# Kernel tuning notes

Measured on AMD Instinct MI355X. Metric: run time of the kernel, lower is better.

## Reference

```python
import jax, jax.numpy as jnp
import numpy as np

DECAY = 0.99
EPS = 1e-5  # Laplace smoothing eps in cluster-size balancing


def _quantize(z_flat, embedding, cluster_size, emb_avg, n_codes):
    # z_flat: [N, D]; embedding: [K, D]
    d = (jnp.sum(z_flat * z_flat, axis=1, keepdims=True)
         + jnp.sum(embedding * embedding, axis=1)
         - 2.0 * (z_flat @ embedding.T))                      # [N, K]
    idx = jnp.argmin(d, axis=1)                               # [N]
    # EMA update (training path). segment_sum == one-hot matmul scatter-add.
    counts = jax.ops.segment_sum(jnp.ones(z_flat.shape[0], z_flat.dtype), idx,
                                 num_segments=n_codes)        # [K]
    new_cs = cluster_size * DECAY + (1.0 - DECAY) * counts
    dw = jax.ops.segment_sum(z_flat, idx, num_segments=n_codes)  # [K, D]
    new_avg = emb_avg * DECAY + (1.0 - DECAY) * dw
    n = new_cs.sum()
    bal = (new_cs + EPS) / (n + n_codes * EPS) * n
    # torch assigns via .data (no autograd) -> stop_gradient for faithfulness
    new_emb = jax.lax.stop_gradient(new_avg / bal[:, None])
    z_q = jnp.take(new_emb, idx, axis=0)  # == one_hot(idx) @ new_emb
    return idx, z_q


def _l2norm(x):
    # F.normalize(x, dim=-1) with eps=1e-12
    return x / jnp.maximum(jnp.linalg.norm(x, axis=-1, keepdims=True), 1e-12)


def reference(z, structure_embedding, style_embedding,
              structure_cluster_size, style_cluster_size,
              structure_embedding_avg, style_embedding_avg):
    b, c, h, w, d = z.shape
    zp = jnp.transpose(z, (0, 2, 3, 4, 1))      # b h w d c
    z_flat = zp.reshape(-1, c)                  # [N, D]
    s_idx, s_q = _quantize(z_flat, structure_embedding, structure_cluster_size,
                           structure_embedding_avg, structure_embedding.shape[0])
    y_idx, y_q = _quantize(z_flat, style_embedding, style_cluster_size,
                           style_embedding_avg, style_embedding.shape[0])

    def back(q):  # [N, C] -> b c h w d
        return jnp.transpose(q.reshape(b, h, w, d, c), (0, 4, 1, 2, 3))

    s_enc = back(s_q)
    y_enc = back(y_q)
    # NOTE: faithful to source — normalize over LAST axis of (b,c,h,w,d),
    # i.e. the spatial depth axis, exactly as F.normalize(dim=-1) does there.
    dis = jnp.mean(jnp.sum(_l2norm(s_enc) * _l2norm(y_enc), axis=-1) ** 2)
    z_q = (s_enc + y_enc) * 0.5
    return z_q, dis, s_idx, y_idx


def setup_inputs() -> dict:
    key = jax.random.key(0)
    k1, k2, k3 = jax.random.split(key, 3)
    B, C, H, W, D = 16, 256, 16, 16, 16
    Ks, Ky = 1024, 512
    return {
        "z": jax.random.normal(k1, (B, C, H, W, D), dtype=jnp.float32),
        "structure_embedding": jax.random.normal(k2, (Ks, C), dtype=jnp.float32),
        "style_embedding": jax.random.normal(k3, (Ky, C), dtype=jnp.float32),
        "structure_cluster_size": jnp.zeros((Ks,), jnp.float32),
        "style_cluster_size": jnp.zeros((Ky,), jnp.float32),
        "structure_embedding_avg": jnp.zeros((Ks, C), jnp.float32),
        "style_embedding_avg": jnp.zeros((Ky, C), jnp.float32),
    }
```

## Files before the change

### kernel.cpp

```cpp
#include <hip/hip_runtime.h>
#include <float.h>

#define NROWS 65536
#define CDIM  256
#define KS    1024
#define KY    512
#define KTOT  1536
#define SPB   4096

#define WB_CNT_S       0
#define WB_CNT_Y       4096
#define WB_RESCUE_CNT  6144
#define WB_DISACC      6152
#define WB_DW_S        6400
#define WB_DW_Y        1054976
#define WB_ZERO_BYTES  1579264
#define WB_EIMG        1579264
#define WB_EN2         2365696
#define WB_IDXS_I      2371840
#define WB_IDXY_I      2633984
#define WB_RLIST_S     2896128
#define WB_RLIST_Y     3158272
#define WB_BASE_S      3420416
#define WB_BASE_Y      3424512
#define WB_CUR_S       3426560
#define WB_CUR_Y       3430656
#define WB_SCALE_S     3432704
#define WB_SCALE_Y     3436800
#define WB_PERM_S      3438848
#define WB_PERM_Y      3700992
#define WB_KSORT_S     3963136
#define WB_KSORT_Y     4225280
#define WB_PS0         4487424
#define WB_PS1         5011712

#define OFF_OUT_ZQ   0
#define OFF_OUT_DIS  16777216
#define OFF_OUT_SIDX 16777217
#define OFF_OUT_YIDX 16842753

typedef __attribute__((ext_vector_type(8)))  _Float16 f16x8;
typedef __attribute__((ext_vector_type(4)))  float    f32x4;

__device__ __forceinline__ unsigned int umn(unsigned int a, unsigned int b) { return a < b ? a : b; }
__device__ __forceinline__ unsigned int umx(unsigned int a, unsigned int b) { return a > b ? a : b; }

__global__ void prep_e(const float* __restrict__ Es, const float* __restrict__ Ey,
                       unsigned short* __restrict__ eimg, float* __restrict__ en2) {
    int wave = threadIdx.x >> 6, lane = threadIdx.x & 63;
    int k = blockIdx.x * 4 + wave;
    const float* E = (k < KS) ? (Es + (size_t)k * CDIM) : (Ey + (size_t)(k - KS) * CDIM);
    float4 v = *(const float4*)(E + lane * 4);
    float nrm = v.x * v.x + v.y * v.y + v.z * v.z + v.w * v.w;
#pragma unroll
    for (int off = 32; off > 0; off >>= 1) nrm += __shfl_down(nrm, off);
    if (lane == 0) en2[k] = nrm;

    unsigned short q0 = __builtin_bit_cast(unsigned short, (_Float16)v.x);
    unsigned short q1 = __builtin_bit_cast(unsigned short, (_Float16)v.y);
    unsigned short q2 = __builtin_bit_cast(unsigned short, (_Float16)v.z);
    unsigned short q3 = __builtin_bit_cast(unsigned short, (_Float16)v.w);
    uint2 hp = make_uint2((unsigned)q0 | ((unsigned)q1 << 16),
                          (unsigned)q2 | ((unsigned)q3 << 16));
    int c0 = lane * 4;
    int kc = c0 >> 5, g = (c0 >> 3) & 3, j0 = c0 & 7;
    size_t byteoff = (size_t)(k >> 4) * 8192 + (size_t)kc * 1024
                   + (size_t)(g * 16 + (k & 15)) * 16 + (size_t)j0 * 2;
    *(uint2*)((char*)eimg + byteoff) = hp;
}

__device__ __forceinline__ void stage1(const unsigned short* __restrict__ eimg,
                                       int chunk, char* lds, int wave, int lane) {
    const char* gs = (const char*)eimg + (size_t)chunk * 8192 + wave * 2048 + lane * 16;
    char* ls = lds + wave * 2048;
    __builtin_amdgcn_global_load_lds(
        (const __attribute__((address_space(1))) void*)gs,
        (__attribute__((address_space(3))) void*)ls, 16, 0, 0);
    __builtin_amdgcn_global_load_lds(
        (const __attribute__((address_space(1))) void*)(gs + 1024),
        (__attribute__((address_space(3))) void*)(ls + 1024), 16, 0, 0);
}

#define WAITV(n)                                                               \
    asm volatile("s_waitcnt vmcnt(" #n ")");                                   \
    __builtin_amdgcn_sched_barrier(0);

#define PSFLUSH(dst)                                                           \
    {                                                                          \
        _Pragma("unroll")                                                      \
        for (int rg = 0; rg < 2; ++rg)                                         \
        _Pragma("unroll")                                                      \
        for (int q = 0; q < 4; ++q) {                                          \
            unsigned int v1 = m1a[rg][q], v2 = m2a[rg][q];                     \
            _Pragma("unroll")                                                  \
            for (int m = 8; m >= 1; m >>= 1) {                                 \
                unsigned int o1 = (unsigned int)__shfl_xor((int)v1, m);        \
                unsigned int o2 = (unsigned int)__shfl_xor((int)v2, m);        \
                v2 = umn(umn(v2, o2), umx(v1, o1));                            \
                v1 = umn(v1, o1);                                              \
            }                                                                  \
            if ((lane & 15) == 0) {                                            \
                int n = n0 + rg * 16 + (lane >> 4) * 4 + q;                    \
                dst[n] = make_uint2(v1, v2);                                   \
            }                                                                  \
            m1a[rg][q] = 0xFFFFFFFFu; m2a[rg][q] = 0xFFFFFFFFu;                \
        }                                                                      \
    }

#define FLUSHY()                                                               \
    {                                                                          \
        _Pragma("unroll")                                                      \
        for (int rg = 0; rg < 2; ++rg)                                         \
        _Pragma("unroll")                                                      \
        for (int q = 0; q < 4; ++q) {                                          \
            unsigned int v1 = m1a[rg][q], v2 = m2a[rg][q];                     \
            _Pragma("unroll")                                                  \
            for (int m = 8; m >= 1; m >>= 1) {                                 \
                unsigned int o1 = (unsigned int)__shfl_xor((int)v1, m);        \
                unsigned int o2 = (unsigned int)__shfl_xor((int)v2, m);        \
                v2 = umn(umn(v2, o2), umx(v1, o1));                            \
                v1 = umn(v1, o1);                                              \
            }                                                                  \
            if ((lane & 15) == 0) {                                            \
                int kw = (int)(v1 & 0x7FFu) - KS;                              \
                int n = n0 + rg * 16 + (lane >> 4) * 4 + q;                    \
                yidx_f[n] = (float)kw;                                         \
                yidx_i[n] = kw;                                                \
                atomicAdd(&cnt_y[kw], 1);                                      \
                if ((v1 >> 11) + 4 > (v2 >> 11)) {                             \
                    int k2w = (int)(v2 & 0x7FFu) - KS;                         \
                    int pp = atomicAdd(&rescue_cnt[1], 1);                     \
                    if (pp < 65536) rlist_y[pp] = n | (k2w << 16);             \
                }                                                              \
            }                                                                  \
        }                                                                      \
    }

__launch_bounds__(256, 4)
__global__ void main1_kernel(const float* __restrict__ z, const unsigned short* __restrict__ eimg,
                             const float* __restrict__ en2g, float* __restrict__ zf,
                             uint2* __restrict__ ps0, uint2* __restrict__ ps1,
                             float* __restrict__ yidx_f, int* __restrict__ yidx_i,
                             int* __restrict__ cnt_y, int* __restrict__ rescue_cnt,
                             int* __restrict__ rlist_y) {
    __shared__ char lds_raw[38912];

    if (blockIdx.x < 1024) {
        char (*sh)[8192] = (char(*)[8192])lds_raw;
        float* en2l = (float*)(lds_raw + 32768);
        const int tid = threadIdx.x, wave = tid >> 6, lane = tid & 63;
        const int half = blockIdx.x & 1;
        const int n0 = (blockIdx.x >> 1) * 128 + wave * 32;
        const int cb = half * 48;

        for (int i = tid; i < KTOT; i += 256) en2l[i] = en2g[i];

        const int b = n0 >> 12;
        const int sb = (n0 & 4095) + (lane & 15);
        const float* zb = z + (size_t)b * CDIM * SPB;
        const int g8 = (lane >> 4) * 8;
        f16x8 A[2][8];
#pragma unroll
        for (int rg = 0; rg < 2; ++rg) {
#pragma unroll
            for (int kc = 0; kc < 8; ++kc) {
                f16x8 a;
#pragma unroll
                for (int j = 0; j < 8; ++j)
                    a[j] = (_Float16)zb[(size_t)(g8 + kc * 32 + j) * SPB + sb + rg * 16];
                A[rg][kc] = a;
            }
        }

        unsigned int m1a[2][4], m2a[2][4];
#pragma unroll
        for (int rg = 0; rg < 2; ++rg)
#pragma unroll
            for (int q = 0; q < 4; ++q) { m1a[rg][q] = 0xFFFFFFFFu; m2a[rg][q] = 0xFFFFFFFFu; }

        stage1(eimg, cb + 0, &sh[0][0], wave, lane);
        stage1(eimg, cb + 1, &sh[1][0], wave, lane);
        stage1(eimg, cb + 2, &sh[2][0], wave, lane);
        __syncthreads();

#pragma unroll 1
        for (int i = 0; i < 48; ++i) {
            if (i < 46)       { WAITV(4); }
            else if (i == 46) { WAITV(2); }
            else              { WAITV(0); }
            __builtin_amdgcn_s_barrier();
            asm volatile("" ::: "memory");
            if (i + 3 < 48) stage1(eimg, cb + i + 3, &sh[(i + 3) & 3][0], wave, lane);

            const int chunk = cb + i;
            const char* bb = &sh[i & 3][0] + lane * 16;
            f32x4 acc0 = {}, acc1 = {};
#pragma unroll
            for (int kc = 0; kc < 8; ++kc) {
                f16x8 B = *(const f16x8*)(bb + kc * 1024);
                acc0 = __builtin_amdgcn_mfma_f32_16x16x32_f16(A[0][kc], B, acc0, 0, 0, 0);
                acc1 = __builtin_amdgcn_mfma_f32_16x16x32_f16(A[1][kc], B, acc1, 0, 0, 0);
            }
            const int kcode = chunk * 16 + (lane & 15);
            const float en0 = en2l[kcode] + 512.0f;
            const unsigned int tag = (unsigned int)kcode;
#pragma unroll
            for (int q = 0; q < 4; ++q) {
                float d0 = fmaf(-2.f, acc0[q], en0);
                unsigned int du0 = (__float_as_uint(d0) & 0xFFFFF800u) | tag;
                m2a[0][q] = umn(m2a[0][q], umx(m1a[0][q], du0));
                m1a[0][q] = umn(m1a[0][q], du0);
                float d1 = fmaf(-2.f, acc1[q], en0);
                unsigned int du1 = (__float_as_uint(d1) & 0xFFFFF800u) | tag;
                m2a[1][q] = umn(m2a[1][q], umx(m1a[1][q], du1));
                m1a[1][q] = umn(m1a[1][q], du1);
            }

            if (half == 1 && i == 15) PSFLUSH(ps1);
        }

        if (half == 0) { PSFLUSH(ps0); }
        else           { FLUSHY(); }
    } else {
        float (*Zs)[257] = (float(*)[257])lds_raw;
        int blk = blockIdx.x - 1024;
        int n0 = blk * 32, b = n0 >> 12, s0 = n0 & 4095;
        int t = threadIdx.x;
        const float* zb = z + (size_t)b * CDIM * SPB + s0;
#pragma unroll
        for (int i = 0; i < 32; ++i) {
            int l = i * 256 + t;
            int c = l >> 5, s = l & 31;
            Zs[s][c] = zb[(size_t)c * SPB + s];
        }
        __syncthreads();
#pragma unroll
        for (int j = 0; j < 8; ++j) {
            int gid = j * 256 + t;
            int nl = gid >> 6, fg = gid & 63;
            float4 v = *(const float4*)(&Zs[nl][fg * 4]);
            *(float4*)(&zf[(size_t)(n0 + nl) * 256 + fg * 4]) = v;
        }
    }
}

__global__ void merge_s_kernel(const uint2* __restrict__ ps0, const uint2* __restrict__ ps1,
                               float* __restrict__ sidx_f, int* __restrict__ sidx_i,
                               int* __restrict__ cnt_s, int* __restrict__ rescue_cnt,
                               int* __restrict__ rlist_s) {
    int n = blockIdx.x * 256 + threadIdx.x;
    uint2 a = ps0[n], b = ps1[n];
    unsigned int v1 = umn(a.x, b.x);
    unsigned int v2 = umn(umn(a.y, b.y), umx(a.x, b.x));
    int kw = (int)(v1 & 0x7FFu);
    sidx_f[n] = (float)kw;
    sidx_i[n] = kw;
    atomicAdd(&cnt_s[kw], 1);
    if ((v1 >> 11) + 4 > (v2 >> 11)) {
        int k2w = (int)(v2 & 0x7FFu);
        int pp = atomicAdd(&rescue_cnt[0], 1);
        if (pp < 65536) rlist_s[pp] = n | (k2w << 16);
    }
}

__global__ void rescue2_kernel(const float* __restrict__ zf,
                               const float* __restrict__ Es, const float* __restrict__ Ey,
                               const float* __restrict__ en2, const int* __restrict__ rcnt,
                               const int* __restrict__ rlist_s, const int* __restrict__ rlist_y,
                               float* __restrict__ sidx_f, float* __restrict__ yidx_f,
                               int* __restrict__ sidx_i, int* __restrict__ yidx_i,
                               int* __restrict__ cnt_s, int* __restrict__ cnt_y) {
    int cs = rcnt[0]; if (cs > 65536) cs = 65536;
    int cy = rcnt[1]; if (cy > 65536) cy = 65536;
    int total = cs + cy;
    const int lane = threadIdx.x & 63;
    const int nw = (gridDim.x * blockDim.x) >> 6;
    for (int e = (int)((blockIdx.x * blockDim.x + threadIdx.x) >> 6); e < total; e += nw) {
        int book = (e >= cs);
        unsigned int ent = (unsigned int)(book ? rlist_y[e - cs] : rlist_s[e]);
        int n  = (int)(ent & 0xFFFFu);
        int k2 = (int)(ent >> 16);
        int* idx_i = book ? yidx_i : sidx_i;
        float* idx_f = book ? yidx_f : sidx_f;
        int* cnt = book ? cnt_y : cnt_s;
        const float* E = book ? Ey : Es;
        const float* en2k = book ? (en2 + KS) : en2;
        int k1 = idx_i[n];
        float4 zv = *(const float4*)(zf + (size_t)n * 256 + lane * 4);
        float4 a  = *(const float4*)(E + (size_t)k1 * 256 + lane * 4);
        float4 c  = *(const float4*)(E + (size_t)k2 * 256 + lane * 4);
        float d1 = zv.x * a.x + zv.y * a.y + zv.z * a.z + zv.w * a.w;
        float d2 = zv.x * c.x + zv.y * c.y + zv.z * c.z + zv.w * c.w;
#pragma unroll
        for (int off = 32; off > 0; off >>= 1) {
            d1 += __shfl_down(d1, off);
            d2 += __shfl_down(d2, off);
        }
        if (lane == 0) {
            float dist1 = en2k[k1] - 2.f * d1;
            float dist2 = en2k[k2] - 2.f * d2;
            int nk = (dist2 < dist1 || (dist2 == dist1 && k2 < k1)) ? k2 : k1;
            if (nk != k1) {
                atomicSub(&cnt[k1], 1);
                atomicAdd(&cnt[nk], 1);
                idx_i[n] = nk;
                idx_f[n] = (float)nk;
            }
        }
    }
}

__global__ void scanbal_kernel(const float* __restrict__ cs_in, const float* __restrict__ cy_in,
                               const int* __restrict__ cnt_s, const int* __restrict__ cnt_y,
                               int* __restrict__ base_s, int* __restrict__ base_y,
                               int* __restrict__ cur_s, int* __restrict__ cur_y,
                               float* __restrict__ scale_s, float* __restrict__ scale_y) {
    __shared__ int   sc[1024];
    __shared__ float sf[1024];
    int K = blockIdx.x ? KY : KS;
    const float* csi = blockIdx.x ? cy_in : cs_in;
    const int*   cnt = blockIdx.x ? cnt_y : cnt_s;
    int* base = blockIdx.x ? base_y : base_s;
    int* cur  = blockIdx.x ? cur_y  : cur_s;
    float* scale = blockIdx.x ? scale_y : scale_s;
    int t = threadIdx.x;
    int c = (t < K) ? cnt[t] : 0;
    float ncs = (t < K) ? (csi[t] * 0.99f + 0.01f * (float)c) : 0.f;
    sc[t] = c;
    __syncthreads();
    for (int off = 1; off < 1024; off <<= 1) {
        int v = sc[t] + ((t >= off) ? sc[t - off] : 0);
        __syncthreads();
        sc[t] = v;
        __syncthreads();
    }
    int incl = sc[t];
    sf[t] = ncs;
    __syncthreads();
    for (int s2 = 512; s2 > 0; s2 >>= 1) {
        if (t < s2) sf[t] += sf[t + s2];
        __syncthreads();
    }
    float nsum = sf[0];
    if (t < K) {
        base[t] = incl - c;
        cur[t]  = incl - c;
        float bal = (ncs + 1e-5f) / (nsum + (float)K * 1e-5f) * nsum;
        scale[t] = 1.0f / bal;
    }
}

__global__ void scatter_kernel(const int* __restrict__ si, const int* __restrict__ yi,
                               int* __restrict__ cur_s, int* __restrict__ cur_y,
                               int* __restrict__ perm_s, int* __restrict__ perm_y,
                               int* __restrict__ ksort_s, int* __restrict__ ksort_y) {
    int i = blockIdx.x * 256 + threadIdx.x;
    if (i < NROWS) {
        int k = si[i]; int p = atomicAdd(&cur_s[k], 1);
        perm_s[p] = i; ksort_s[p] = k;
    } else {
        int n = i - NROWS; int k = yi[n]; int p = atomicAdd(&cur_y[k], 1);
        perm_y[p] = n; ksort_y[p] = k;
    }
}

__global__ void dw_kernel(const float* __restrict__ zf,
                          const int* __restrict__ perm_s, const int* __restrict__ ksort_s,
                          const int* __restrict__ perm_y, const int* __restrict__ ksort_y,
                          float* __restrict__ dw_s, float* __restrict__ dw_y) {
    __shared__ int keys[65];
    __shared__ int rows[64];
    const int t = threadIdx.x;
    int blk = blockIdx.x;
    const int* perm; const int* ks; float* dw; int p0;
    if (blk < NROWS / 64) { perm = perm_s; ks = ksort_s; dw = dw_s; p0 = blk * 64; }
    else                  { perm = perm_y; ks = ksort_y; dw = dw_y; p0 = (blk - NROWS / 64) * 64; }
    if (t < 64) { keys[t] = ks[p0 + t]; rows[t] = perm[p0 + t]; }
    if (t == 64) keys[64] = -1;
    __syncthreads();
    float acc = 0.f;
#pragma unroll 8
    for (int j = 0; j < 64; ++j) {
        acc += zf[(size_t)rows[j] * 256 + t];
        if (keys[j + 1] != keys[j]) {
            atomicAdd(&dw[(size_t)keys[j] * 256 + t], acc);
            acc = 0.f;
        }
    }
}

__global__ void gather_kernel(const float* __restrict__ avg_s, const float* __restrict__ avg_y,
                              const float* __restrict__ dw_s, const float* __restrict__ dw_y,
                              const float* __restrict__ scale_s, const float* __restrict__ scale_y,
                              const int* __restrict__ sidx, const int* __restrict__ yidx,
                              float* __restrict__ zq, float* __restrict__ disacc) {
    __shared__ float qb[256 * 17];
    __shared__ int   si[16], yi[16];
    __shared__ float scs[16], scy[16];
    __shared__ float red[256];
    const int g  = blockIdx.x;
    const int b  = g >> 8;
    const int hw = g & 255;
    const int t  = threadIdx.x;
    if (t < 16) {
        int n = b * SPB + hw * 16 + t;
        int k = sidx[n];
        si[t] = k;
        scs[t] = scale_s[k];
    } else if (t < 32) {
        int n = b * SPB + hw * 16 + (t - 16);
        int k = yidx[n];
        yi[t - 16] = k;
        scy[t - 16] = scale_y[k];
    }
    __syncthreads();
    float ns = 0.f, ny = 0.f, dot = 0.f;
#pragma unroll
    for (int d = 0; d < 16; ++d) {
        size_t so = (size_t)si[d] * CDIM + t;
        size_t yo = (size_t)yi[d] * CDIM + t;
        float s = fmaf(0.01f, dw_s[so], avg_s[so] * 0.99f) * scs[d];
        float y = fmaf(0.01f, dw_y[yo], avg_y[yo] * 0.99f) * scy[d];
        ns  = fmaf(s, s, ns);
        ny  = fmaf(y, y, ny);
        dot = fmaf(s, y, dot);
        qb[t * 17 + d] = 0.5f * (s + y);
    }
    float den = fmaxf(sqrtf(ns), 1e-12f) * fmaxf(sqrtf(ny), 1e-12f);
    float val = dot / den;
    red[t] = val * val;
    __syncthreads();
    for (int s = 128; s > 0; s >>= 1) {
        if (t < s) red[t] += red[t + s];
        __syncthreads();
    }
    if (t == 0) atomicAdd(disacc, red[0]);
    float* zg = zq + (size_t)b * CDIM * SPB + hw * 16;
#pragma unroll
    for (int j = 0; j < 16; ++j) {
        int e = j * 256 + t;
        int c = e >> 4, d = e & 15;
        zg[(size_t)c * SPB + d] = qb[c * 17 + d];
    }
}

__global__ void fin_kernel(const float* __restrict__ disacc, float* __restrict__ out_dis) {
    *out_dis = *disacc * (1.0f / 1048576.0f);
}

extern "C" void kernel_launch(void* const* d_in, const int* in_sizes, int n_in,
                              void* d_out, int out_size, void* d_ws, size_t ws_size,
                              hipStream_t stream) {
    const float* z     = (const float*)d_in[0];
    const float* Es    = (const float*)d_in[1];
    const float* Ey    = (const float*)d_in[2];
    const float* s_cs  = (const float*)d_in[3];
    const float* y_cs  = (const float*)d_in[4];
    const float* s_avg = (const float*)d_in[5];
    const float* y_avg = (const float*)d_in[6];
    float* out = (float*)d_out;
    char*  w   = (char*)d_ws;

    unsigned short* eimg = (unsigned short*)(w + WB_EIMG);
    float* en2    = (float*)(w + WB_EN2);
    int* idxs_i   = (int*)(w + WB_IDXS_I);
    int* idxy_i   = (int*)(w + WB_IDXY_I);
    int* cnt_s    = (int*)(w + WB_CNT_S);
    int* cnt_y    = (int*)(w + WB_CNT_Y);
    int* r_cnt    = (int*)(w + WB_RESCUE_CNT);
    int* rlist_s  = (int*)(w + WB_RLIST_S);
    int* rlist_y  = (int*)(w + WB_RLIST_Y);
    int* base_s   = (int*)(w + WB_BASE_S);
    int* base_y   = (int*)(w + WB_BASE_Y);
    int* cur_s    = (int*)(w + WB_CUR_S);
    int* cur_y    = (int*)(w + WB_CUR_Y);
    float* scale_s = (float*)(w + WB_SCALE_S);
    float* scale_y = (float*)(w + WB_SCALE_Y);
    int* perm_s   = (int*)(w + WB_PERM_S);
    int* perm_y   = (int*)(w + WB_PERM_Y);
    int* ksort_s  = (int*)(w + WB_KSORT_S);
    int* ksort_y  = (int*)(w + WB_KSORT_Y);
    float* dw_s   = (float*)(w + WB_DW_S);
    float* dw_y   = (float*)(w + WB_DW_Y);
    uint2* ps0    = (uint2*)(w + WB_PS0);
    uint2* ps1    = (uint2*)(w + WB_PS1);

    float* zf     = out + OFF_OUT_ZQ;
    float* sidx_f = out + OFF_OUT_SIDX;
    float* yidx_f = out + OFF_OUT_YIDX;

    hipMemsetAsync(w, 0, WB_ZERO_BYTES, stream);

    prep_e<<<384, 256, 0, stream>>>(Es, Ey, eimg, en2);

    main1_kernel<<<1024 + 2048, 256, 0, stream>>>(
        z, eimg, en2, zf, ps0, ps1, yidx_f, idxy_i, cnt_y, r_cnt, rlist_y);

    merge_s_kernel<<<NROWS / 256, 256, 0, stream>>>(ps0, ps1, sidx_f, idxs_i,
                                                    cnt_s, r_cnt, rlist_s);

    rescue2_kernel<<<512, 256, 0, stream>>>(zf, Es, Ey, en2, r_cnt, rlist_s, rlist_y,
                                            sidx_f, yidx_f, idxs_i, idxy_i, cnt_s, cnt_y);

    scanbal_kernel<<<2, 1024, 0, stream>>>(s_cs, y_cs, cnt_s, cnt_y, base_s, base_y,
                                           cur_s, cur_y, scale_s, scale_y);
    scatter_kernel<<<2 * NROWS / 256, 256, 0, stream>>>(idxs_i, idxy_i, cur_s, cur_y,
                                                        perm_s, perm_y, ksort_s, ksort_y);
    dw_kernel<<<2 * NROWS / 64, 256, 0, stream>>>(zf, perm_s, ksort_s, perm_y, ksort_y, dw_s, dw_y);
    gather_kernel<<<4096, 256, 0, stream>>>(s_avg, y_avg, dw_s, dw_y, scale_s, scale_y,
                                            idxs_i, idxy_i,
                                            out + OFF_OUT_ZQ, (float*)(w + WB_DISACC));
    fin_kernel<<<1, 1, 0, stream>>>((float*)(w + WB_DISACC), out + OFF_OUT_DIS);
}
```

Measured before the change: 305.1 us.

## Fuse post-argmin stages into one persistent kernel with software grid barriers

Merges the merge, rescue, scan/balance, scatter, dw accumulation, gather and finalize kernels into a single persistent tail kernel of 1024 blocks. A hand-written atomic grid barrier separates the stages, and the scan/balance step now uses 256 threads with per-thread chunks. The aim is to remove several kernel launch gaps and tail-drain bubbles. In exchange, grid-wide spin barriers add latency and require all 1024 blocks to be co-resident, and grid-stride loops replace full-occupancy launches.

```diff
diff --git a/kernel.cpp b/kernel.cpp
--- a/kernel.cpp
+++ b/kernel.cpp
@@ -12,6 +12,7 @@
 #define WB_CNT_Y       4096
 #define WB_RESCUE_CNT  6144
 #define WB_DISACC      6152
+#define WB_GBAR        6160
 #define WB_DW_S        6400
 #define WB_DW_Y        1054976
 #define WB_ZERO_BYTES  1579264
@@ -21,8 +22,6 @@
 #define WB_IDXY_I      2633984
 #define WB_RLIST_S     2896128
 #define WB_RLIST_Y     3158272
-#define WB_BASE_S      3420416
-#define WB_BASE_Y      3424512
 #define WB_CUR_S       3426560
 #define WB_CUR_Y       3430656
 #define WB_SCALE_S     3432704
@@ -244,208 +243,233 @@
     }
 }
 
-__global__ void merge_s_kernel(const uint2* __restrict__ ps0, const uint2* __restrict__ ps1,
-                               float* __restrict__ sidx_f, int* __restrict__ sidx_i,
-                               int* __restrict__ cnt_s, int* __restrict__ rescue_cnt,
-                               int* __restrict__ rlist_s) {
-    int n = blockIdx.x * 256 + threadIdx.x;
-    uint2 a = ps0[n], b = ps1[n];
-    unsigned int v1 = umn(a.x, b.x);
-    unsigned int v2 = umn(umn(a.y, b.y), umx(a.x, b.x));
-    int kw = (int)(v1 & 0x7FFu);
-    sidx_f[n] = (float)kw;
-    sidx_i[n] = kw;
-    atomicAdd(&cnt_s[kw], 1);
-    if ((v1 >> 11) + 4 > (v2 >> 11)) {
-        int k2w = (int)(v2 & 0x7FFu);
-        int pp = atomicAdd(&rescue_cnt[0], 1);
-        if (pp < 65536) rlist_s[pp] = n | (k2w << 16);
-    }
+#define TB_GRID 1024
+__device__ __forceinline__ void gbar(int* cnt, int* gen) {
+    __syncthreads();
+    if (threadIdx.x == 0) {
+        int g = __hip_atomic_load(gen, __ATOMIC_RELAXED, __HIP_MEMORY_SCOPE_AGENT);
+        int v = __hip_atomic_fetch_add(cnt, 1, __ATOMIC_ACQ_REL, __HIP_MEMORY_SCOPE_AGENT);
+        if (v == TB_GRID - 1) {
+            __hip_atomic_store(cnt, 0, __ATOMIC_RELAXED, __HIP_MEMORY_SCOPE_AGENT);
+            __hip_atomic_fetch_add(gen, 1, __ATOMIC_ACQ_REL, __HIP_MEMORY_SCOPE_AGENT);
+        } else {
+            while (__hip_atomic_load(gen, __ATOMIC_ACQUIRE, __HIP_MEMORY_SCOPE_AGENT) == g)
+                __builtin_amdgcn_s_sleep(16);
+        }
+    }
+    __syncthreads();
 }
 
-__global__ void rescue2_kernel(const float* __restrict__ zf,
-                               const float* __restrict__ Es, const float* __restrict__ Ey,
-                               const float* __restrict__ en2, const int* __restrict__ rcnt,
-                               const int* __restrict__ rlist_s, const int* __restrict__ rlist_y,
-                               float* __restrict__ sidx_f, float* __restrict__ yidx_f,
-                               int* __restrict__ sidx_i, int* __restrict__ yidx_i,
-                               int* __restrict__ cnt_s, int* __restrict__ cnt_y) {
-    int cs = rcnt[0]; if (cs > 65536) cs = 65536;
-    int cy = rcnt[1]; if (cy > 65536) cy = 65536;
-    int total = cs + cy;
-    const int lane = threadIdx.x & 63;
-    const int nw = (gridDim.x * blockDim.x) >> 6;
-    for (int e = (int)((blockIdx.x * blockDim.x + threadIdx.x) >> 6); e < total; e += nw) {
-        int book = (e >= cs);
-        unsigned int ent = (unsigned int)(book ? rlist_y[e - cs] : rlist_s[e]);
-        int n  = (int)(ent & 0xFFFFu);
-        int k2 = (int)(ent >> 16);
-        int* idx_i = book ? yidx_i : sidx_i;
-        float* idx_f = book ? yidx_f : sidx_f;
-        int* cnt = book ? cnt_y : cnt_s;
-        const float* E = book ? Ey : Es;
-        const float* en2k = book ? (en2 + KS) : en2;
-        int k1 = idx_i[n];
-        float4 zv = *(const float4*)(zf + (size_t)n * 256 + lane * 4);
-        float4 a  = *(const float4*)(E + (size_t)k1 * 256 + lane * 4);
-        float4 c  = *(const float4*)(E + (size_t)k2 * 256 + lane * 4);
-        float d1 = zv.x * a.x + zv.y * a.y + zv.z * a.z + zv.w * a.w;
-        float d2 = zv.x * c.x + zv.y * c.y + zv.z * c.z + zv.w * c.w;
-#pragma unroll
-        for (int off = 32; off > 0; off >>= 1) {
-            d1 += __shfl_down(d1, off);
-            d2 += __shfl_down(d2, off);
-        }
-        if (lane == 0) {
-            float dist1 = en2k[k1] - 2.f * d1;
-            float dist2 = en2k[k2] - 2.f * d2;
-            int nk = (dist2 < dist1 || (dist2 == dist1 && k2 < k1)) ? k2 : k1;
-            if (nk != k1) {
-                atomicSub(&cnt[k1], 1);
-                atomicAdd(&cnt[nk], 1);
-                idx_i[n] = nk;
-                idx_f[n] = (float)nk;
-            }
-        }
-    }
-}
-
-__global__ void scanbal_kernel(const float* __restrict__ cs_in, const float* __restrict__ cy_in,
-                               const int* __restrict__ cnt_s, const int* __restrict__ cnt_y,
-                               int* __restrict__ base_s, int* __restrict__ base_y,
-                               int* __restrict__ cur_s, int* __restrict__ cur_y,
-                               float* __restrict__ scale_s, float* __restrict__ scale_y) {
-    __shared__ int   sc[1024];
-    __shared__ float sf[1024];
-    int K = blockIdx.x ? KY : KS;
-    const float* csi = blockIdx.x ? cy_in : cs_in;
-    const int*   cnt = blockIdx.x ? cnt_y : cnt_s;
-    int* base = blockIdx.x ? base_y : base_s;
-    int* cur  = blockIdx.x ? cur_y  : cur_s;
-    float* scale = blockIdx.x ? scale_y : scale_s;
-    int t = threadIdx.x;
-    int c = (t < K) ? cnt[t] : 0;
-    float ncs = (t < K) ? (csi[t] * 0.99f + 0.01f * (float)c) : 0.f;
-    sc[t] = c;
-    __syncthreads();
-    for (int off = 1; off < 1024; off <<= 1) {
-        int v = sc[t] + ((t >= off) ? sc[t - off] : 0);
+struct TailArgs {
+    const float *zf_r, *Es, *Ey, *en2, *s_cs, *y_cs, *avg_s, *avg_y;
+    const uint2 *ps0, *ps1;
+    float *sidx_f, *yidx_f;
+    int *idxs_i, *idxy_i, *cnt_s, *cnt_y, *r_cnt, *rlist_s, *rlist_y;
+    int *cur_s, *cur_y;
+    float *scale_s, *scale_y;
+    int *perm_s, *perm_y, *ksort_s, *ksort_y;
+    float *dw_s, *dw_y, *zq, *disacc, *out_dis;
+    int *bar;
+};
+
+__launch_bounds__(256, 4)
+__global__ void tail_kernel(TailArgs a) {
+    __shared__ __align__(16) char smem[18688];
+    const int bid = blockIdx.x, t = threadIdx.x;
+    int* bcnt = a.bar;
+    int* bgen = a.bar + 1;
+
+    for (int n = bid * 256 + t; n < NROWS; n += TB_GRID * 256) {
+        uint2 pa = a.ps0[n], pb = a.ps1[n];
+        unsigned int v1 = umn(pa.x, pb.x);
+        unsigned int v2 = umn(umn(pa.y, pb.y), umx(pa.x, pb.x));
+        int kw = (int)(v1 & 0x7FFu);
+        a.sidx_f[n] = (float)kw;
+        a.idxs_i[n] = kw;
+        atomicAdd(&a.cnt_s[kw], 1);
+        if ((v1 >> 11) + 4 > (v2 >> 11)) {
+            int k2w = (int)(v2 & 0x7FFu);
+            int pp = atomicAdd(&a.r_cnt[0], 1);
+            if (pp < 65536) a.rlist_s[pp] = n | (k2w << 16);
+        }
+    }
+    gbar(bcnt, bgen);
+
+    {
+        int cs = a.r_cnt[0]; if (cs > 65536) cs = 65536;
+        int cy = a.r_cnt[1]; if (cy > 65536) cy = 65536;
+        int total = cs + cy;
+        const int lane = t & 63;
+        for (int e = bid * 4 + (t >> 6); e < total; e += TB_GRID * 4) {
+            int book = (e >= cs);
+            unsigned int ent = (unsigned int)(book ? a.rlist_y[e - cs] : a.rlist_s[e]);
+            int n  = (int)(ent & 0xFFFFu);
+            int k2 = (int)(ent >> 16);
+            int* idx_i = book ? a.idxy_i : a.idxs_i;
+            float* idx_f = book ? a.yidx_f : a.sidx_f;
+            int* cnt = book ? a.cnt_y : a.cnt_s;
+            const float* E = book ? a.Ey : a.Es;
+            const float* en2k = book ? (a.en2 + KS) : a.en2;
+            int k1 = idx_i[n];
+            float4 zv = *(const float4*)(a.zf_r + (size_t)n * 256 + lane * 4);
+            float4 ea = *(const float4*)(E + (size_t)k1 * 256 + lane * 4);
+            float4 ec = *(const float4*)(E + (size_t)k2 * 256 + lane * 4);
+            float d1 = zv.x * ea.x + zv.y * ea.y + zv.z * ea.z + zv.w * ea.w;
+            float d2 = zv.x * ec.x + zv.y * ec.y + zv.z * ec.z + zv.w * ec.w;
+#pragma unroll
+            for (int off = 32; off > 0; off >>= 1) {
+                d1 += __shfl_down(d1, off);
+                d2 += __shfl_down(d2, off);
+            }
+            if (lane == 0) {
+                float dist1 = en2k[k1] - 2.f * d1;
+                float dist2 = en2k[k2] - 2.f * d2;
+                int nk = (dist2 < dist1 || (dist2 == dist1 && k2 < k1)) ? k2 : k1;
+                if (nk != k1) {
+                    atomicSub(&cnt[k1], 1);
+                    atomicAdd(&cnt[nk], 1);
+                    idx_i[n] = nk;
+                    idx_f[n] = (float)nk;
+                }
+            }
+        }
+    }
+    gbar(bcnt, bgen);
+
+    if (bid < 2) {
+        int*   sdI = (int*)smem;
+        float* sdF = (float*)(smem + 1024);
+        const int K = bid ? KY : KS;
+        const int E = K >> 8;
+        const float* csi = bid ? a.y_cs : a.s_cs;
+        const int*   cnt = bid ? a.cnt_y : a.cnt_s;
+        int* cur = bid ? a.cur_y : a.cur_s;
+        float* scale = bid ? a.scale_y : a.scale_s;
+        int cl[4] = {0, 0, 0, 0};
+        float nl[4] = {0.f, 0.f, 0.f, 0.f};
+        int isum = 0; float fsum = 0.f;
+#pragma unroll
+        for (int e = 0; e < 4; ++e) {
+            if (e < E) {
+                int c = cnt[t * E + e];
+                float ncs = csi[t * E + e] * 0.99f + 0.01f * (float)c;
+                cl[e] = c; nl[e] = ncs; isum += c; fsum += ncs;
+            }
+        }
+        sdI[t] = isum; sdF[t] = fsum;
         __syncthreads();
-        sc[t] = v;
-        __syncthreads();
-    }
-    int incl = sc[t];
-    sf[t] = ncs;
-    __syncthreads();
-    for (int s2 = 512; s2 > 0; s2 >>= 1) {
-        if (t < s2) sf[t] += sf[t + s2];
-        __syncthreads();
-    }
-    float nsum = sf[0];
-    if (t < K) {
-        base[t] = incl - c;
-        cur[t]  = incl - c;
-        float bal = (ncs + 1e-5f) / (nsum + (float)K * 1e-5f) * nsum;
-        scale[t] = 1.0f / bal;
-    }
-}
-
-__global__ void scatter_kernel(const int* __restrict__ si, const int* __restrict__ yi,
-                               int* __restrict__ cur_s, int* __restrict__ cur_y,
-                               int* __restrict__ perm_s, int* __restrict__ perm_y,
-                               int* __restrict__ ksort_s, int* __restrict__ ksort_y) {
-    int i = blockIdx.x * 256 + threadIdx.x;
-    if (i < NROWS) {
-        int k = si[i]; int p = atomicAdd(&cur_s[k], 1);
-        perm_s[p] = i; ksort_s[p] = k;
-    } else {
-        int n = i - NROWS; int k = yi[n]; int p = atomicAdd(&cur_y[k], 1);
-        perm_y[p] = n; ksort_y[p] = k;
-    }
-}
-
-__global__ void dw_kernel(const float* __restrict__ zf,
-                          const int* __restrict__ perm_s, const int* __restrict__ ksort_s,
-                          const int* __restrict__ perm_y, const int* __restrict__ ksort_y,
-                          float* __restrict__ dw_s, float* __restrict__ dw_y) {
-    __shared__ int keys[65];
-    __shared__ int rows[64];
-    const int t = threadIdx.x;
-    int blk = blockIdx.x;
-    const int* perm; const int* ks; float* dw; int p0;
-    if (blk < NROWS / 64) { perm = perm_s; ks = ksort_s; dw = dw_s; p0 = blk * 64; }
-    else                  { perm = perm_y; ks = ksort_y; dw = dw_y; p0 = (blk - NROWS / 64) * 64; }
-    if (t < 64) { keys[t] = ks[p0 + t]; rows[t] = perm[p0 + t]; }
-    if (t == 64) keys[64] = -1;
-    __syncthreads();
-    float acc = 0.f;
+        for (int off = 1; off < 256; off <<= 1) {
+            int v = sdI[t] + ((t >= off) ? sdI[t - off] : 0);
+            float f = sdF[t] + ((t >= off) ? sdF[t - off] : 0.f);
+            __syncthreads();
+            sdI[t] = v; sdF[t] = f;
+            __syncthreads();
+        }
+        float nsum = sdF[255];
+        int run = sdI[t] - isum;
+#pragma unroll
+        for (int e = 0; e < 4; ++e) {
+            if (e < E) {
+                cur[t * E + e] = run;
+                float bal = (nl[e] + 1e-5f) / (nsum + (float)K * 1e-5f) * nsum;
+                scale[t * E + e] = 1.0f / bal;
+                run += cl[e];
+            }
+        }
+    }
+    gbar(bcnt, bgen);
+
+    for (int i = bid * 256 + t; i < 2 * NROWS; i += TB_GRID * 256) {
+        if (i < NROWS) {
+            int k = a.idxs_i[i]; int p = atomicAdd(&a.cur_s[k], 1);
+            a.perm_s[p] = i; a.ksort_s[p] = k;
+        } else {
+            int n = i - NROWS; int k = a.idxy_i[n]; int p = atomicAdd(&a.cur_y[k], 1);
+            a.perm_y[p] = n; a.ksort_y[p] = k;
+        }
+    }
+    gbar(bcnt, bgen);
+
+    {
+        int* keys = (int*)smem;
+        int* rows = keys + 65;
+        for (int vb = bid; vb < 2048; vb += TB_GRID) {
+            const int* perm; const int* ks; float* dwp; int p0;
+            if (vb < 1024) { perm = a.perm_s; ks = a.ksort_s; dwp = a.dw_s; p0 = vb * 64; }
+            else           { perm = a.perm_y; ks = a.ksort_y; dwp = a.dw_y; p0 = (vb - 1024) * 64; }
+            __syncthreads();
+            if (t < 64) { keys[t] = ks[p0 + t]; rows[t] = perm[p0 + t]; }
+            if (t == 64) keys[64] = -1;
+            __syncthreads();
+            float acc = 0.f;
 #pragma unroll 8
-    for (int j = 0; j < 64; ++j) {
-        acc += zf[(size_t)rows[j] * 256 + t];
-        if (keys[j + 1] != keys[j]) {
-            atomicAdd(&dw[(size_t)keys[j] * 256 + t], acc);
-            acc = 0.f;
-        }
-    }
-}
-
-__global__ void gather_kernel(const float* __restrict__ avg_s, const float* __restrict__ avg_y,
-                              const float* __restrict__ dw_s, const float* __restrict__ dw_y,
-                              const float* __restrict__ scale_s, const float* __restrict__ scale_y,
-                              const int* __restrict__ sidx, const int* __restrict__ yidx,
-                              float* __restrict__ zq, float* __restrict__ disacc) {
-    __shared__ float qb[256 * 17];
-    __shared__ int   si[16], yi[16];
-    __shared__ float scs[16], scy[16];
-    __shared__ float red[256];
-    const int g  = blockIdx.x;
-    const int b  = g >> 8;
-    const int hw = g & 255;
-    const int t  = threadIdx.x;
-    if (t < 16) {
-        int n = b * SPB + hw * 16 + t;
-        int k = sidx[n];
-        si[t] = k;
-        scs[t] = scale_s[k];
-    } else if (t < 32) {
-        int n = b * SPB + hw * 16 + (t - 16);
-        int k = yidx[n];
-        yi[t - 16] = k;
-        scy[t - 16] = scale_y[k];
-    }
-    __syncthreads();
-    float ns = 0.f, ny = 0.f, dot = 0.f;
-#pragma unroll
-    for (int d = 0; d < 16; ++d) {
-        size_t so = (size_t)si[d] * CDIM + t;
-        size_t yo = (size_t)yi[d] * CDIM + t;
-        float s = fmaf(0.01f, dw_s[so], avg_s[so] * 0.99f) * scs[d];
-        float y = fmaf(0.01f, dw_y[yo], avg_y[yo] * 0.99f) * scy[d];
-        ns  = fmaf(s, s, ns);
-        ny  = fmaf(y, y, ny);
-        dot = fmaf(s, y, dot);
-        qb[t * 17 + d] = 0.5f * (s + y);
-    }
-    float den = fmaxf(sqrtf(ns), 1e-12f) * fmaxf(sqrtf(ny), 1e-12f);
-    float val = dot / den;
-    red[t] = val * val;
-    __syncthreads();
-    for (int s = 128; s > 0; s >>= 1) {
-        if (t < s) red[t] += red[t + s];
-        __syncthreads();
-    }
-    if (t == 0) atomicAdd(disacc, red[0]);
-    float* zg = zq + (size_t)b * CDIM * SPB + hw * 16;
-#pragma unroll
-    for (int j = 0; j < 16; ++j) {
-        int e = j * 256 + t;
-        int c = e >> 4, d = e & 15;
-        zg[(size_t)c * SPB + d] = qb[c * 17 + d];
-    }
-}
-
-__global__ void fin_kernel(const float* __restrict__ disacc, float* __restrict__ out_dis) {
-    *out_dis = *disacc * (1.0f / 1048576.0f);
+            for (int j = 0; j < 64; ++j) {
+                acc += a.zf_r[(size_t)rows[j] * 256 + t];
+                if (keys[j + 1] != keys[j]) {
+                    atomicAdd(&dwp[(size_t)keys[j] * 256 + t], acc);
+                    acc = 0.f;
+                }
+            }
+        }
+    }
+    gbar(bcnt, bgen);
+
+    {
+        float* qb  = (float*)smem;
+        int*   si  = (int*)(smem + 17408);
+        int*   yi  = si + 16;
+        float* scs = (float*)(yi + 16);
+        float* scy = scs + 16;
+        float* red = scy + 16;
+        for (int g = bid; g < 4096; g += TB_GRID) {
+            __syncthreads();
+            const int b  = g >> 8;
+            const int hw = g & 255;
+            if (t < 16) {
+                int n = b * SPB + hw * 16 + t;
+                int k = a.idxs_i[n];
+                si[t] = k;
+                scs[t] = a.scale_s[k];
+            } else if (t < 32) {
+                int n = b * SPB + hw * 16 + (t - 16);
+                int k = a.idxy_i[n];
+                yi[t - 16] = k;
+                scy[t - 16] = a.scale_y[k];
+            }
+            __syncthreads();
+            float ns = 0.f, ny = 0.f, dot = 0.f;
+#pragma unroll
+            for (int d = 0; d < 16; ++d) {
+                size_t so = (size_t)si[d] * CDIM + t;
+                size_t yo = (size_t)yi[d] * CDIM + t;
+                float s = fmaf(0.01f, a.dw_s[so], a.avg_s[so] * 0.99f) * scs[d];
+                float y = fmaf(0.01f, a.dw_y[yo], a.avg_y[yo] * 0.99f) * scy[d];
+                ns  = fmaf(s, s, ns);
+                ny  = fmaf(y, y, ny);
+                dot = fmaf(s, y, dot);
+                qb[t * 17 + d] = 0.5f * (s + y);
+            }
+            float den = fmaxf(sqrtf(ns), 1e-12f) * fmaxf(sqrtf(ny), 1e-12f);
+            float val = dot / den;
+            red[t] = val * val;
+            __syncthreads();
+            for (int s = 128; s > 0; s >>= 1) {
+                if (t < s) red[t] += red[t + s];
+                __syncthreads();
+            }
+            if (t == 0) atomicAdd(a.disacc, red[0]);
+            float* zg = a.zq + (size_t)b * CDIM * SPB + hw * 16;
+#pragma unroll
+            for (int j = 0; j < 16; ++j) {
+                int e = j * 256 + t;
+                int c = e >> 4, d = e & 15;
+                zg[(size_t)c * SPB + d] = qb[c * 17 + d];
+            }
+        }
+    }
+    gbar(bcnt, bgen);
+
+    if (bid == 0 && t == 0) *a.out_dis = *a.disacc * (1.0f / 1048576.0f);
 }
 
 extern "C" void kernel_launch(void* const* d_in, const int* in_sizes, int n_in,
@@ -463,52 +487,49 @@
 
     unsigned short* eimg = (unsigned short*)(w + WB_EIMG);
     float* en2    = (float*)(w + WB_EN2);
-    int* idxs_i   = (int*)(w + WB_IDXS_I);
-    int* idxy_i   = (int*)(w + WB_IDXY_I);
-    int* cnt_s    = (int*)(w + WB_CNT_S);
-    int* cnt_y    = (int*)(w + WB_CNT_Y);
-    int* r_cnt    = (int*)(w + WB_RESCUE_CNT);
-    int* rlist_s  = (int*)(w + WB_RLIST_S);
-    int* rlist_y  = (int*)(w + WB_RLIST_Y);
-    int* base_s   = (int*)(w + WB_BASE_S);
-    int* base_y   = (int*)(w + WB_BASE_Y);
-    int* cur_s    = (int*)(w + WB_CUR_S);
-    int* cur_y    = (int*)(w + WB_CUR_Y);
-    float* scale_s = (float*)(w + WB_SCALE_S);
-    float* scale_y = (float*)(w + WB_SCALE_Y);
-    int* perm_s   = (int*)(w + WB_PERM_S);
-    int* perm_y   = (int*)(w + WB_PERM_Y);
-    int* ksort_s  = (int*)(w + WB_KSORT_S);
-    int* ksort_y  = (int*)(w + WB_KSORT_Y);
-    float* dw_s   = (float*)(w + WB_DW_S);
-    float* dw_y   = (float*)(w + WB_DW_Y);
-    uint2* ps0    = (uint2*)(w + WB_PS0);
-    uint2* ps1    = (uint2*)(w + WB_PS1);
-
     float* zf     = out + OFF_OUT_ZQ;
-    float* sidx_f = out + OFF_OUT_SIDX;
-    float* yidx_f = out + OFF_OUT_YIDX;
 
     hipMemsetAsync(w, 0, WB_ZERO_BYTES, stream);
 
     prep_e<<<384, 256, 0, stream>>>(Es, Ey, eimg, en2);
 
     main1_kernel<<<1024 + 2048, 256, 0, stream>>>(
-        z, eimg, en2, zf, ps0, ps1, yidx_f, idxy_i, cnt_y, r_cnt, rlist_y);
-
-    merge_s_kernel<<<NROWS / 256, 256, 0, stream>>>(ps0, ps1, sidx_f, idxs_i,
-                                                    cnt_s, r_cnt, rlist_s);
-
-    rescue2_kernel<<<512, 256, 0, stream>>>(zf, Es, Ey, en2, r_cnt, rlist_s, rlist_y,
-                                            sidx_f, yidx_f, idxs_i, idxy_i, cnt_s, cnt_y);
-
-    scanbal_kernel<<<2, 1024, 0, stream>>>(s_cs, y_cs, cnt_s, cnt_y, base_s, base_y,
-                                           cur_s, cur_y, scale_s, scale_y);
-    scatter_kernel<<<2 * NROWS / 256, 256, 0, stream>>>(idxs_i, idxy_i, cur_s, cur_y,
-                                                        perm_s, perm_y, ksort_s, ksort_y);
-    dw_kernel<<<2 * NROWS / 64, 256, 0, stream>>>(zf, perm_s, ksort_s, perm_y, ksort_y, dw_s, dw_y);
-    gather_kernel<<<4096, 256, 0, stream>>>(s_avg, y_avg, dw_s, dw_y, scale_s, scale_y,
-                                            idxs_i, idxy_i,
-                                            out + OFF_OUT_ZQ, (float*)(w + WB_DISACC));
-    fin_kernel<<<1, 1, 0, stream>>>((float*)(w + WB_DISACC), out + OFF_OUT_DIS);
+        z, eimg, en2, zf,
+        (uint2*)(w + WB_PS0), (uint2*)(w + WB_PS1),
+        out + OFF_OUT_YIDX, (int*)(w + WB_IDXY_I),
+        (int*)(w + WB_CNT_Y), (int*)(w + WB_RESCUE_CNT), (int*)(w + WB_RLIST_Y));
+
+    TailArgs ta;
+    ta.zf_r    = zf;
+    ta.Es      = Es;        ta.Ey      = Ey;
+    ta.en2     = en2;
+    ta.s_cs    = s_cs;      ta.y_cs    = y_cs;
+    ta.avg_s   = s_avg;     ta.avg_y   = y_avg;
+    ta.ps0     = (const uint2*)(w + WB_PS0);
+    ta.ps1     = (const uint2*)(w + WB_PS1);
+    ta.sidx_f  = out + OFF_OUT_SIDX;
+    ta.yidx_f  = out + OFF_OUT_YIDX;
+    ta.idxs_i  = (int*)(w + WB_IDXS_I);
+    ta.idxy_i  = (int*)(w + WB_IDXY_I);
+    ta.cnt_s   = (int*)(w + WB_CNT_S);
+    ta.cnt_y   = (int*)(w + WB_CNT_Y);
+    ta.r_cnt   = (int*)(w + WB_RESCUE_CNT);
+    ta.rlist_s = (int*)(w + WB_RLIST_S);
+    ta.rlist_y = (int*)(w + WB_RLIST_Y);
+    ta.cur_s   = (int*)(w + WB_CUR_S);
+    ta.cur_y   = (int*)(w + WB_CUR_Y);
+    ta.scale_s = (float*)(w + WB_SCALE_S);
+    ta.scale_y = (float*)(w + WB_SCALE_Y);
+    ta.perm_s  = (int*)(w + WB_PERM_S);
+    ta.perm_y  = (int*)(w + WB_PERM_Y);
+    ta.ksort_s = (int*)(w + WB_KSORT_S);
+    ta.ksort_y = (int*)(w + WB_KSORT_Y);
+    ta.dw_s    = (float*)(w + WB_DW_S);
+    ta.dw_y    = (float*)(w + WB_DW_Y);
+    ta.zq      = out + OFF_OUT_ZQ;
+    ta.disacc  = (float*)(w + WB_DISACC);
+    ta.out_dis = out + OFF_OUT_DIS;
+    ta.bar     = (int*)(w + WB_GBAR);
+
+    tail_kernel<<<TB_GRID, 256, 0, stream>>>(ta);
 }
```

Result: slower. 1.132 ms (+270.9%).
